# Kernel optimization log

Measured on AMD Instinct MI355X. Metric: run time of the kernel, lower is better.

Reference implementation:

```python
import jax, jax.numpy as jnp
import numpy as np

NUM_NODES = 10000
NUM_EDGES = 160000
NUM_REL = 4
IN_DIM = 15
HID = 512
NUM_GRAPHS = 64


def setup_inputs() -> dict:
    key = jax.random.key(0)
    ks = jax.random.split(key, 8)
    x = jax.random.normal(ks[0], (NUM_NODES, IN_DIM), dtype=jnp.float32)
    edge_index = jax.random.randint(ks[1], (2, NUM_EDGES), 0, NUM_NODES, dtype=jnp.int64)
    edge_type = jax.random.randint(ks[2], (NUM_EDGES,), 0, NUM_REL, dtype=jnp.int64)
    batch = jnp.sort(jax.random.randint(ks[3], (NUM_NODES,), 0, NUM_GRAPHS, dtype=jnp.int64))
    # glorot-style scaled params
    W1_rel = jax.random.normal(ks[4], (NUM_REL, IN_DIM, HID), dtype=jnp.float32) * (1.0 / np.sqrt(IN_DIM))
    W1_root = jax.random.normal(ks[5], (IN_DIM, HID), dtype=jnp.float32) * (1.0 / np.sqrt(IN_DIM))
    b1 = jnp.zeros((HID,), dtype=jnp.float32)
    W2_rel = jax.random.normal(ks[6], (NUM_REL, HID, HID), dtype=jnp.float32) * (1.0 / np.sqrt(HID))
    W2_root = jax.random.normal(ks[7], (HID, HID), dtype=jnp.float32) * (1.0 / np.sqrt(HID))
    b2 = jnp.zeros((HID,), dtype=jnp.float32)
    return {"x": x, "edge_index": edge_index, "edge_type": edge_type, "batch": batch,
            "W1_rel": W1_rel, "W1_root": W1_root, "b1": b1,
            "W2_rel": W2_rel, "W2_root": W2_root, "b2": b2}


def _rgcn_conv(x, src, tgt, seg, W_rel, W_root, b):
    """PyG RGCNConv (non-decomposed, aggr='mean'):
    out[i] = x[i]@W_root + b + sum_r (mean_{j in N_r(i)} x[j]) @ W_r.
    seg = tgt*NUM_REL + edge_type combines (target, relation) into one segment id
    so a single segment_sum handles the per-relation mean."""
    E = src.shape[0]
    msgs = x[src]                                              # [E, d_in] irregular gather
    sums = jax.ops.segment_sum(msgs, seg, num_segments=x.shape[0] * NUM_REL)
    cnts = jax.ops.segment_sum(jnp.ones((E,), x.dtype), seg, num_segments=x.shape[0] * NUM_REL)
    mean = sums / jnp.maximum(cnts, 1.0)[:, None]              # [N*R, d_in]
    mean = mean.reshape(x.shape[0], NUM_REL, x.shape[1])       # [N, R, d_in]
    return jnp.einsum('nrd,rdo->no', mean, W_rel) + x @ W_root + b


def reference(x, edge_index, edge_type, batch, W1_rel, W1_root, b1, W2_rel, W2_root, b2):
    src, tgt = edge_index[0], edge_index[1]
    seg = tgt * NUM_REL + edge_type
    h = jax.nn.relu(_rgcn_conv(x, src, tgt, seg, W1_rel, W1_root, b1))
    h = jax.nn.relu(_rgcn_conv(h, src, tgt, seg, W2_rel, W2_root, b2))
    # global_mean_pool over graphs
    gsum = jax.ops.segment_sum(h, batch, num_segments=NUM_GRAPHS)
    gcnt = jax.ops.segment_sum(jnp.ones((h.shape[0],), h.dtype), batch, num_segments=NUM_GRAPHS)
    return gsum / jnp.maximum(gcnt, 1.0)[:, None]              # [NUM_GRAPHS, HID]
```

## Files before the change

kernel.cpp:

```cpp
#include <hip/hip_runtime.h>

#define N_NODES 10000
#define N_EDGES 160000
#define N_REL 4
#define IN_DIM 15
#define HID 512
#define N_GRAPHS 64
#define NSEG (N_NODES * N_REL)
#define K2 (N_REL * HID + HID)
#define MAXC 64

typedef __attribute__((ext_vector_type(8))) short s16x8;
typedef __attribute__((ext_vector_type(4))) float f32x4;

__device__ __forceinline__ float bf2f(short s) {
    return __uint_as_float(((unsigned)(unsigned short)s) << 16);
}
__device__ __forceinline__ short f2bf(float f) {
    unsigned u = __float_as_uint(f);
    u += 0x7fff + ((u >> 16) & 1);
    return (short)(u >> 16);
}

#define B_CNT    0u
#define B_ELIST  160000u
#define B_H      10400000u
#define B_MEAN2  20640000u
#define B_BT     61600000u

__global__ void bin_kernel(const int* __restrict__ src, const int* __restrict__ tgt,
                           const int* __restrict__ et, int* __restrict__ cnt,
                           int* __restrict__ elist, float* __restrict__ out) {
    int e = blockIdx.x * blockDim.x + threadIdx.x;
    if (e < N_GRAPHS * HID) out[e] = 0.f;
    if (e >= N_EDGES) return;
    int seg = tgt[e] * N_REL + et[e];
    int pos = atomicAdd(&cnt[seg], 1);
    if (pos < MAXC) elist[seg * MAXC + pos] = src[e];
}

#define NPB 16
__global__ __launch_bounds__(512) void layer1_kernel(
        const float* __restrict__ x, const int* __restrict__ cnts,
        const int* __restrict__ elist,
        const float* __restrict__ W1_rel, const float* __restrict__ W1_root,
        const float* __restrict__ b1, short* __restrict__ h) {
    const int nb = blockIdx.x * NPB;
    __shared__ float f[NPB][76];
    const int t = threadIdx.x;
    for (int task = t; task < NPB * 60; task += 512) {
        int m = task / 60, k = task - m * 60;
        int n = nb + m;
        int seg = n * N_REL + k / IN_DIM;
        int d = k % IN_DIM;
        int cnt = cnts[seg]; if (cnt > MAXC) cnt = MAXC;
        int b = seg * MAXC;
        float acc = 0.f;
        for (int i = 0; i < cnt; ++i) acc += x[elist[b + i] * IN_DIM + d];
        f[m][k] = (cnt > 0) ? acc / (float)cnt : 0.f;
    }
    for (int task = t; task < NPB * 16; task += 512) {
        int m = task >> 4, d = task & 15;
        f[m][60 + d] = (d < IN_DIM) ? x[(nb + m) * IN_DIM + d] : 0.f;
    }
    __syncthreads();
    const int o = t;
    float acc[NPB];
    const float bias = b1[o];
    #pragma unroll
    for (int m = 0; m < NPB; ++m) acc[m] = bias;
    #pragma unroll 2
    for (int k4 = 0; k4 < 76; k4 += 4) {
        float w0, w1, w2, w3;
        if (k4 < 56) {
            w0 = W1_rel[(k4 + 0) * HID + o];
            w1 = W1_rel[(k4 + 1) * HID + o];
            w2 = W1_rel[(k4 + 2) * HID + o];
            w3 = W1_rel[(k4 + 3) * HID + o];
        } else if (k4 == 56) {
            w0 = W1_rel[56 * HID + o];
            w1 = W1_rel[57 * HID + o];
            w2 = W1_rel[58 * HID + o];
            w3 = W1_rel[59 * HID + o];
        } else if (k4 < 72) {
            w0 = W1_root[(k4 - 60 + 0) * HID + o];
            w1 = W1_root[(k4 - 60 + 1) * HID + o];
            w2 = W1_root[(k4 - 60 + 2) * HID + o];
            w3 = W1_root[(k4 - 60 + 3) * HID + o];
        } else {
            w0 = W1_root[12 * HID + o];
            w1 = W1_root[13 * HID + o];
            w2 = W1_root[14 * HID + o];
            w3 = 0.f;
        }
        #pragma unroll
        for (int m = 0; m < NPB; ++m) {
            float4 fv = *(const float4*)&f[m][k4];
            acc[m] = fmaf(fv.x, w0, fmaf(fv.y, w1, fmaf(fv.z, w2, fmaf(fv.w, w3, acc[m]))));
        }
    }
    #pragma unroll
    for (int m = 0; m < NPB; ++m)
        h[(long)(nb + m) * HID + o] = f2bf(fmaxf(acc[m], 0.0f));
}

#define MEAN2_BLOCKS (NSEG / 4)
__global__ __launch_bounds__(256) void mean2_wtrans_kernel(
        const short* __restrict__ h, const int* __restrict__ cnts,
        const int* __restrict__ elist, short* __restrict__ mean2,
        const float* __restrict__ W2_rel, const float* __restrict__ W2_root,
        short* __restrict__ Bt) {
    __shared__ float tile[64][65];
    if (blockIdx.x < MEAN2_BLOCKS) {
        const int wid = (blockIdx.x << 2) + (threadIdx.x >> 6);
        const int lane = threadIdx.x & 63;
        int cnt = cnts[wid]; if (cnt > MAXC) cnt = MAXC;
        const int b = wid * MAXC;
        float acc[8] = {0.f,0.f,0.f,0.f,0.f,0.f,0.f,0.f};
        int el = 0;
        if (lane < cnt) el = elist[b + lane];
        for (int i = 0; i < cnt; ++i) {
            int row = __shfl(el, i, 64);
            const s16x8 v = *(const s16x8*)(h + (long)row * HID + lane * 8);
            #pragma unroll
            for (int j = 0; j < 8; ++j) acc[j] += bf2f(v[j]);
        }
        const float inv = (cnt > 0) ? 1.0f / (float)cnt : 0.0f;
        s16x8 o;
        #pragma unroll
        for (int j = 0; j < 8; ++j) o[j] = f2bf(acc[j] * inv);
        *(s16x8*)(mean2 + (long)wid * HID + lane * 8) = o;
    } else {
        const int bx = blockIdx.x - MEAN2_BLOCKS;
        const int k0 = (bx % 40) * 64;
        const int o0 = (bx / 40) * 64;
        const int t = threadIdx.x;
        #pragma unroll
        for (int i = 0; i < 16; ++i) {
            int idx = t + i * 256;
            int kk = idx >> 6, oo = idx & 63;
            int k = k0 + kk;
            float v = (k < N_REL * HID) ? W2_rel[(long)k * HID + o0 + oo]
                                        : W2_root[(long)(k - N_REL * HID) * HID + o0 + oo];
            tile[kk][oo] = v;
        }
        __syncthreads();
        #pragma unroll
        for (int i = 0; i < 16; ++i) {
            int idx = t + i * 256;
            int oo = idx >> 6, kk = idx & 63;
            Bt[(long)(o0 + oo) * K2 + k0 + kk] = f2bf(tile[kk][oo]);
        }
    }
}

#define GM 64
#define GN 128
#define GK 64
#define NT (K2 / GK)
#define NWG (4 * ((N_NODES + GM - 1) / GM))
__global__ __launch_bounds__(256) void gemm2_kernel(
        const short* __restrict__ mean2, const short* __restrict__ h,
        const short* __restrict__ Bt, const float* __restrict__ b2,
        const int* __restrict__ batch, float* __restrict__ out) {
    __shared__ __align__(16) short Al[2][GM * GK];
    __shared__ __align__(16) short Bl[2][GN * GK];
    const int tid = threadIdx.x;
    const int lane = tid & 63;
    const int w = tid >> 6;
    const int orig = blockIdx.x;
    const int q = NWG >> 3, r = NWG & 7;
    const int xcd = orig & 7, cidx = orig >> 3;
    const int wgid = (xcd < r ? xcd * (q + 1) : r * (q + 1) + (xcd - r) * q) + cidx;
    const int m0 = (wgid >> 2) * GM;
    const int n0 = (wgid & 3) * GN;
    const int l15 = lane & 15, lg = lane >> 4;

    f32x4 acc[4][2];
    #pragma unroll
    for (int a = 0; a < 4; ++a)
        #pragma unroll
        for (int bb = 0; bb < 2; ++bb)
            acc[a][bb] = (f32x4){0.f, 0.f, 0.f, 0.f};

#define STAGE(buf, k0)                                                           \
    {                                                                            \
        _Pragma("unroll")                                                        \
        for (int i = 0; i < 2; ++i) {                                            \
            int c = tid + i * 256;                                               \
            int row = c >> 3, slot = c & 7;                                      \
            int srcslot = slot ^ (row & 7);                                      \
            int n = m0 + row; if (n > N_NODES - 1) n = N_NODES - 1;              \
            int kg = (k0) + srcslot * 8;                                         \
            const short* gsrc = (kg < N_REL * HID)                               \
                ? (mean2 + (long)n * (N_REL * HID) + kg)                         \
                : (h + (long)n * HID + (kg - N_REL * HID));                      \
            __builtin_amdgcn_global_load_lds(                                    \
                (const __attribute__((address_space(1))) void*)gsrc,             \
                (__attribute__((address_space(3))) void*)(Al[buf] + c * 8),      \
                16, 0, 0);                                                       \
        }                                                                        \
        _Pragma("unroll")                                                        \
        for (int i = 0; i < 4; ++i) {                                            \
            int c = tid + i * 256;                                               \
            int row = c >> 3, slot = c & 7;                                      \
            int srcslot = slot ^ (row & 7);                                      \
            const short* gsrc = Bt + (long)(n0 + row) * K2 + (k0) + srcslot * 8; \
            __builtin_amdgcn_global_load_lds(                                    \
                (const __attribute__((address_space(1))) void*)gsrc,             \
                (__attribute__((address_space(3))) void*)(Bl[buf] + c * 8),      \
                16, 0, 0);                                                       \
        }                                                                        \
    }

    STAGE(0, 0);
    asm volatile("s_waitcnt vmcnt(0)" ::: "memory");
    __builtin_amdgcn_s_barrier();
    asm volatile("" ::: "memory");

    int cur = 0;
    #pragma unroll 1
    for (int t = 0; t < NT; ++t) {
        if (t + 1 < NT) STAGE(cur ^ 1, (t + 1) * GK);
        #pragma unroll
        for (int hh = 0; hh < 2; ++hh) {
            s16x8 af[4], bfr[2];
            #pragma unroll
            for (int fm = 0; fm < 4; ++fm) {
                int row = fm * 16 + l15;
                int slot = (hh * 4 + lg) ^ (row & 7);
                af[fm] = *(const s16x8*)(Al[cur] + row * GK + slot * 8);
            }
            #pragma unroll
            for (int fn = 0; fn < 2; ++fn) {
                int row = w * 32 + fn * 16 + l15;
                int slot = (hh * 4 + lg) ^ (row & 7);
                bfr[fn] = *(const s16x8*)(Bl[cur] + row * GK + slot * 8);
            }
            #pragma unroll
            for (int fm = 0; fm < 4; ++fm)
                #pragma unroll
                for (int fn = 0; fn < 2; ++fn)
                    asm("v_mfma_f32_16x16x32_bf16 %0, %1, %2, %0"
                        : "+v"(acc[fm][fn]) : "v"(af[fm]), "v"(bfr[fn]));
        }
        asm volatile("s_waitcnt vmcnt(0)" ::: "memory");
        __builtin_amdgcn_s_barrier();
        asm volatile("" ::: "memory");
        cur ^= 1;
    }
#undef STAGE

    const int col0 = n0 + w * 32 + l15;
    const float bias0 = b2[col0];
    const float bias1 = b2[col0 + 16];
    int cur_g = -1;
    float s0 = 0.f, s1 = 0.f;
    #pragma unroll
    for (int fm = 0; fm < 4; ++fm) {
        #pragma unroll
        for (int r2 = 0; r2 < 4; ++r2) {
            int n = m0 + fm * 16 + 4 * lg + r2;
            if (n < N_NODES) {
                int g = batch[n];
                if (g != cur_g) {
                    if (cur_g >= 0) {
                        float* og = out + (long)cur_g * HID;
                        atomicAdd(og + col0,      s0);
                        atomicAdd(og + col0 + 16, s1);
                    }
                    cur_g = g; s0 = 0.f; s1 = 0.f;
                }
                s0 += fmaxf(acc[fm][0][r2] + bias0, 0.f);
                s1 += fmaxf(acc[fm][1][r2] + bias1, 0.f);
            }
        }
    }
    if (cur_g >= 0) {
        float* og = out + (long)cur_g * HID;
        atomicAdd(og + col0,      s0);
        atomicAdd(og + col0 + 16, s1);
    }
}

__global__ __launch_bounds__(256) void pool_fin_kernel(const int* __restrict__ batch,
                                                       float* __restrict__ out) {
    const int g = blockIdx.x;
    const int t = threadIdx.x;
    int s, e;
    { int l = 0, hsz = N_NODES;
      while (l < hsz) { int m = (l + hsz) >> 1; if (batch[m] < g) l = m + 1; else hsz = m; }
      s = l; }
    { int l = s, hsz = N_NODES;
      while (l < hsz) { int m = (l + hsz) >> 1; if (batch[m] < g + 1) l = m + 1; else hsz = m; }
      e = l; }
    const float inv = (e > s) ? 1.0f / (float)(e - s) : 0.f;
    out[g * HID + t * 2]     *= inv;
    out[g * HID + t * 2 + 1] *= inv;
}

extern "C" void kernel_launch(void* const* d_in, const int* in_sizes, int n_in,
                              void* d_out, int out_size, void* d_ws, size_t ws_size,
                              hipStream_t stream) {
    const float* x       = (const float*)d_in[0];
    const int*   ei      = (const int*)d_in[1];
    const int*   src     = ei;
    const int*   tgt     = ei + N_EDGES;
    const int*   etype   = (const int*)d_in[2];
    const int*   batch   = (const int*)d_in[3];
    const float* W1_rel  = (const float*)d_in[4];
    const float* W1_root = (const float*)d_in[5];
    const float* b1      = (const float*)d_in[6];
    const float* W2_rel  = (const float*)d_in[7];
    const float* W2_root = (const float*)d_in[8];
    const float* b2      = (const float*)d_in[9];
    float* out = (float*)d_out;

    char* ws = (char*)d_ws;
    int*   cnts  = (int*)(ws + B_CNT);
    int*   elist = (int*)(ws + B_ELIST);
    short* h     = (short*)(ws + B_H);
    short* mean2 = (short*)(ws + B_MEAN2);
    short* Bt    = (short*)(ws + B_BT);

    hipMemsetAsync(cnts, 0, NSEG * sizeof(int), stream);

    bin_kernel<<<(N_EDGES + 255) / 256, 256, 0, stream>>>(src, tgt, etype,
                                                          cnts, elist, out);

    layer1_kernel<<<N_NODES / NPB, 512, 0, stream>>>(x, cnts, elist,
                                                     W1_rel, W1_root, b1, h);

    mean2_wtrans_kernel<<<MEAN2_BLOCKS + (K2 / 64) * (HID / 64), 256, 0, stream>>>(
        h, cnts, elist, mean2, W2_rel, W2_root, Bt);

    gemm2_kernel<<<NWG, 256, 0, stream>>>(mean2, h, Bt, b2, batch, out);

    pool_fin_kernel<<<N_GRAPHS, 256, 0, stream>>>(batch, out);
}
```

Baseline: 129.7 us.

## Fold pooling normalization into GEMM epilogue and prepack layer-1 weights as bf16

Per-graph inverse counts are now computed inside the binning kernel and applied in the GEMM epilogue before the atomic adds, so the separate pool finalization kernel and its launch go away. The binning kernel also packs W1_rel and W1_root into an interleaved bf16 buffer, letting layer 1 load four weights with one 8-byte load instead of four strided fp32 loads. This rounds the layer-1 weights to bf16, which adds some precision loss.

Result: faster. 125.0 us (-3.7%).

```diff
diff --git a/kernel.cpp b/kernel.cpp
--- a/kernel.cpp
+++ b/kernel.cpp
@@ -11,6 +11,7 @@
 #define MAXC 64
 
 typedef __attribute__((ext_vector_type(8))) short s16x8;
+typedef __attribute__((ext_vector_type(4))) short s16x4;
 typedef __attribute__((ext_vector_type(4))) float f32x4;
 
 __device__ __forceinline__ float bf2f(short s) {
@@ -24,15 +25,45 @@
 
 #define B_CNT    0u
 #define B_ELIST  160000u
-#define B_H      10400000u
-#define B_MEAN2  20640000u
-#define B_BT     61600000u
+#define B_GINV   10400000u
+#define B_W1B    10400256u
+#define B_H      10478080u
+#define B_MEAN2  20718080u
+#define B_BT     61678080u
 
 __global__ void bin_kernel(const int* __restrict__ src, const int* __restrict__ tgt,
-                           const int* __restrict__ et, int* __restrict__ cnt,
-                           int* __restrict__ elist, float* __restrict__ out) {
+                           const int* __restrict__ et, const int* __restrict__ batch,
+                           const float* __restrict__ W1_rel, const float* __restrict__ W1_root,
+                           int* __restrict__ cnt, int* __restrict__ elist,
+                           float* __restrict__ out, float* __restrict__ ginv,
+                           short* __restrict__ W1b) {
     int e = blockIdx.x * blockDim.x + threadIdx.x;
     if (e < N_GRAPHS * HID) out[e] = 0.f;
+    if (e < N_GRAPHS) {
+        int g = e;
+        int s, en;
+        { int l = 0, hsz = N_NODES;
+          while (l < hsz) { int m = (l + hsz) >> 1; if (batch[m] < g) l = m + 1; else hsz = m; }
+          s = l; }
+        { int l = s, hsz = N_NODES;
+          while (l < hsz) { int m = (l + hsz) >> 1; if (batch[m] < g + 1) l = m + 1; else hsz = m; }
+          en = l; }
+        ginv[g] = (en > s) ? 1.0f / (float)(en - s) : 0.f;
+    }
+    if (e < 19 * 512) {
+        int gidx = e >> 9, o = e & 511;
+        short w[4];
+        #pragma unroll
+        for (int j = 0; j < 4; ++j) {
+            int k = gidx * 4 + j;
+            float v;
+            if (k < 60)      v = W1_rel[(long)k * HID + o];
+            else if (k < 75) v = W1_root[(long)(k - 60) * HID + o];
+            else             v = 0.f;
+            w[j] = f2bf(v);
+        }
+        *(s16x4*)(W1b + (long)e * 4) = *(s16x4*)w;
+    }
     if (e >= N_EDGES) return;
     int seg = tgt[e] * N_REL + et[e];
     int pos = atomicAdd(&cnt[seg], 1);
@@ -42,8 +73,7 @@
 #define NPB 16
 __global__ __launch_bounds__(512) void layer1_kernel(
         const float* __restrict__ x, const int* __restrict__ cnts,
-        const int* __restrict__ elist,
-        const float* __restrict__ W1_rel, const float* __restrict__ W1_root,
+        const int* __restrict__ elist, const short* __restrict__ W1b,
         const float* __restrict__ b1, short* __restrict__ h) {
     const int nb = blockIdx.x * NPB;
     __shared__ float f[NPB][76];
@@ -71,28 +101,8 @@
     for (int m = 0; m < NPB; ++m) acc[m] = bias;
     #pragma unroll 2
     for (int k4 = 0; k4 < 76; k4 += 4) {
-        float w0, w1, w2, w3;
-        if (k4 < 56) {
-            w0 = W1_rel[(k4 + 0) * HID + o];
-            w1 = W1_rel[(k4 + 1) * HID + o];
-            w2 = W1_rel[(k4 + 2) * HID + o];
-            w3 = W1_rel[(k4 + 3) * HID + o];
-        } else if (k4 == 56) {
-            w0 = W1_rel[56 * HID + o];
-            w1 = W1_rel[57 * HID + o];
-            w2 = W1_rel[58 * HID + o];
-            w3 = W1_rel[59 * HID + o];
-        } else if (k4 < 72) {
-            w0 = W1_root[(k4 - 60 + 0) * HID + o];
-            w1 = W1_root[(k4 - 60 + 1) * HID + o];
-            w2 = W1_root[(k4 - 60 + 2) * HID + o];
-            w3 = W1_root[(k4 - 60 + 3) * HID + o];
-        } else {
-            w0 = W1_root[12 * HID + o];
-            w1 = W1_root[13 * HID + o];
-            w2 = W1_root[14 * HID + o];
-            w3 = 0.f;
-        }
+        s16x4 wv = *(const s16x4*)(W1b + (long)((k4 >> 2) * 512 + o) * 4);
+        float w0 = bf2f(wv[0]), w1 = bf2f(wv[1]), w2 = bf2f(wv[2]), w3 = bf2f(wv[3]);
         #pragma unroll
         for (int m = 0; m < NPB; ++m) {
             float4 fv = *(const float4*)&f[m][k4];
@@ -162,7 +172,8 @@
 __global__ __launch_bounds__(256) void gemm2_kernel(
         const short* __restrict__ mean2, const short* __restrict__ h,
         const short* __restrict__ Bt, const float* __restrict__ b2,
-        const int* __restrict__ batch, float* __restrict__ out) {
+        const int* __restrict__ batch, const float* __restrict__ ginv,
+        float* __restrict__ out) {
     __shared__ __align__(16) short Al[2][GM * GK];
     __shared__ __align__(16) short Bl[2][GN * GK];
     const int tid = threadIdx.x;
@@ -265,9 +276,10 @@
                 int g = batch[n];
                 if (g != cur_g) {
                     if (cur_g >= 0) {
+                        float gi = ginv[cur_g];
                         float* og = out + (long)cur_g * HID;
-                        atomicAdd(og + col0,      s0);
-                        atomicAdd(og + col0 + 16, s1);
+                        atomicAdd(og + col0,      s0 * gi);
+                        atomicAdd(og + col0 + 16, s1 * gi);
                     }
                     cur_g = g; s0 = 0.f; s1 = 0.f;
                 }
@@ -277,26 +289,11 @@
         }
     }
     if (cur_g >= 0) {
+        float gi = ginv[cur_g];
         float* og = out + (long)cur_g * HID;
-        atomicAdd(og + col0,      s0);
-        atomicAdd(og + col0 + 16, s1);
-    }
-}
-
-__global__ __launch_bounds__(256) void pool_fin_kernel(const int* __restrict__ batch,
-                                                       float* __restrict__ out) {
-    const int g = blockIdx.x;
-    const int t = threadIdx.x;
-    int s, e;
-    { int l = 0, hsz = N_NODES;
-      while (l < hsz) { int m = (l + hsz) >> 1; if (batch[m] < g) l = m + 1; else hsz = m; }
-      s = l; }
-    { int l = s, hsz = N_NODES;
-      while (l < hsz) { int m = (l + hsz) >> 1; if (batch[m] < g + 1) l = m + 1; else hsz = m; }
-      e = l; }
-    const float inv = (e > s) ? 1.0f / (float)(e - s) : 0.f;
-    out[g * HID + t * 2]     *= inv;
-    out[g * HID + t * 2 + 1] *= inv;
+        atomicAdd(og + col0,      s0 * gi);
+        atomicAdd(og + col0 + 16, s1 * gi);
+    }
 }
 
 extern "C" void kernel_launch(void* const* d_in, const int* in_sizes, int n_in,
@@ -319,22 +316,21 @@
     char* ws = (char*)d_ws;
     int*   cnts  = (int*)(ws + B_CNT);
     int*   elist = (int*)(ws + B_ELIST);
+    float* ginv  = (float*)(ws + B_GINV);
+    short* W1b   = (short*)(ws + B_W1B);
     short* h     = (short*)(ws + B_H);
     short* mean2 = (short*)(ws + B_MEAN2);
     short* Bt    = (short*)(ws + B_BT);
 
     hipMemsetAsync(cnts, 0, NSEG * sizeof(int), stream);
 
-    bin_kernel<<<(N_EDGES + 255) / 256, 256, 0, stream>>>(src, tgt, etype,
-                                                          cnts, elist, out);
-
-    layer1_kernel<<<N_NODES / NPB, 512, 0, stream>>>(x, cnts, elist,
-                                                     W1_rel, W1_root, b1, h);
+    bin_kernel<<<(N_EDGES + 255) / 256, 256, 0, stream>>>(
+        src, tgt, etype, batch, W1_rel, W1_root, cnts, elist, out, ginv, W1b);
+
+    layer1_kernel<<<N_NODES / NPB, 512, 0, stream>>>(x, cnts, elist, W1b, b1, h);
 
     mean2_wtrans_kernel<<<MEAN2_BLOCKS + (K2 / 64) * (HID / 64), 256, 0, stream>>>(
         h, cnts, elist, mean2, W2_rel, W2_root, Bt);
 
-    gemm2_kernel<<<NWG, 256, 0, stream>>>(mean2, h, Bt, b2, batch, out);
-
-    pool_fin_kernel<<<N_GRAPHS, 256, 0, stream>>>(batch, out);
-}
+    gemm2_kernel<<<NWG, 256, 0, stream>>>(mean2, h, Bt, b2, batch, ginv, out);
+}
```
